# Kernel tuning notes

Hardware: AMD Instinct MI355X
Metric: run time of the kernel (lower is better)

The kernel has to match this reference:

```python
import jax, jax.numpy as jnp
import numpy as np
from functools import partial

EPS = 1e-5
SCALE = 2
NUM_BLOCKS = 2


def _layernorm(x, g, b):
    mu = jnp.mean(x, axis=-1, keepdims=True)
    var = jnp.var(x, axis=-1, keepdims=True)
    return (x - mu) * jax.lax.rsqrt(var + EPS) * g + b


def _rwkv(tokens, td, Wk, Wv, Wr, Wo, ln_g, ln_b):
    # tokens: (B, N, C)
    x = _layernorm(tokens, ln_g, ln_b)
    k = jnp.einsum('bnc,oc->bno', x, Wk)
    v = jnp.einsum('bnc,oc->bno', x, Wv)
    r = jax.nn.sigmoid(jnp.einsum('bnc,oc->bno', x, Wr))
    decay = jnp.exp(-jax.nn.relu(td))  # (C,)

    def step(state, inp):
        kt, vt, rt = inp  # each (B, C)
        state = state * decay + kt
        return state, rt * (state + vt)

    B, N, C = tokens.shape
    init = jnp.zeros((B, C), dtype=tokens.dtype)
    # scan over token axis
    _, yT = jax.lax.scan(step, init, (k.transpose(1, 0, 2), v.transpose(1, 0, 2), r.transpose(1, 0, 2)))
    y = yT.transpose(1, 0, 2)  # (B, N, C)
    return jnp.einsum('bnc,oc->bno', y, Wo)


def reference(x, global_state, cond_gw, cond_gb, cond_bw, cond_bb,
              td, Wk, Wv, Wr, Wo, ln_g, ln_b, gp_w, gp_b, bp_w, bp_b):
    B, C, H, W = x.shape
    Hp, Wp = H * SCALE, W * SCALE
    # bilinear upsample, half-pixel centers == torch align_corners=False
    x_up = jax.image.resize(x, (B, C, Hp, Wp), method='bilinear')
    tokens = x_up.reshape(B, C, Hp * Wp).transpose(0, 2, 1)  # (B, N, C)
    # semantic conditioning (FiLM from global state)
    gamma = (global_state @ cond_gw.T + cond_gb)[:, None, :]
    beta = (global_state @ cond_bw.T + cond_bb)[:, None, :]
    tokens = tokens * (1.0 + gamma) + beta

    out = x_up
    cur = tokens
    for i in range(NUM_BLOCKS):
        if i > 0:
            cur = out.reshape(B, C, Hp * Wp).transpose(0, 2, 1)
        t = _rwkv(cur, td[i], Wk[i], Wv[i], Wr[i], Wo[i], ln_g[i], ln_b[i])
        g = jnp.einsum('bnc,oc->bno', t, gp_w[i]) + gp_b[i]
        bt = jnp.einsum('bnc,oc->bno', t, bp_w[i]) + bp_b[i]
        g = g.transpose(0, 2, 1).reshape(B, C, Hp, Wp)
        bt = bt.transpose(0, 2, 1).reshape(B, C, Hp, Wp)
        out = out * (1.0 + jnp.tanh(g)) + bt
    return out


def setup_inputs() -> dict:
    key = jax.random.key(0)
    ks = jax.random.split(key, 16)
    B, C, H, W = 8, 128, 64, 64
    w_scale = 0.02
    inp = {
        'x': jax.random.normal(ks[0], (B, C, H, W), jnp.float32),
        'global_state': jax.random.normal(ks[1], (B, C), jnp.float32),
        'cond_gw': jax.random.normal(ks[2], (C, C), jnp.float32) * w_scale,
        'cond_gb': jnp.zeros((C,), jnp.float32),
        'cond_bw': jax.random.normal(ks[3], (C, C), jnp.float32) * w_scale,
        'cond_bb': jnp.zeros((C,), jnp.float32),
        'td': jax.random.uniform(ks[4], (NUM_BLOCKS, C), jnp.float32),
        'Wk': jax.random.normal(ks[5], (NUM_BLOCKS, C, C), jnp.float32) * w_scale,
        'Wv': jax.random.normal(ks[6], (NUM_BLOCKS, C, C), jnp.float32) * w_scale,
        'Wr': jax.random.normal(ks[7], (NUM_BLOCKS, C, C), jnp.float32) * w_scale,
        'Wo': jax.random.normal(ks[8], (NUM_BLOCKS, C, C), jnp.float32) * w_scale,
        'ln_g': jnp.ones((NUM_BLOCKS, C), jnp.float32),
        'ln_b': jnp.zeros((NUM_BLOCKS, C), jnp.float32),
        'gp_w': jax.random.normal(ks[9], (NUM_BLOCKS, C, C), jnp.float32) * w_scale,
        'gp_b': jnp.zeros((NUM_BLOCKS, C), jnp.float32),
        'bp_w': jax.random.normal(ks[10], (NUM_BLOCKS, C, C), jnp.float32) * w_scale,
        'bp_b': jnp.zeros((NUM_BLOCKS, C), jnp.float32),
    }
    return inp
```

## Files before the change

kernel.cpp:

```cpp
#include <hip/hip_runtime.h>
#include <hip/hip_bf16.h>

#define BB 8
#define CC 128
#define NN 16384
#define MM (BB * NN)
#define NCH 64
#define CLN 256

typedef __attribute__((ext_vector_type(8))) short short8;
typedef __attribute__((ext_vector_type(4))) float floatx4;
typedef unsigned short u16;
typedef unsigned int u32;

__device__ __forceinline__ float bf2f(u16 h) {
  u32 u = ((u32)h) << 16;
  return __builtin_bit_cast(float, u);
}
__device__ __forceinline__ u16 f2bf(float f) {
  u32 u = __builtin_bit_cast(u32, f);
  u32 r = u + 0x7FFFu + ((u >> 16) & 1u);
  return (u16)(r >> 16);
}

__global__ void film_kernel(const float* __restrict__ gs, const float* __restrict__ gw,
                            const float* __restrict__ gb, const float* __restrict__ bw,
                            const float* __restrict__ bb, float* __restrict__ gamma,
                            float* __restrict__ beta) {
  int idx = blockIdx.x * 256 + threadIdx.x;
  int b = idx >> 7, c = idx & 127;
  float sg = 0.f, sb = 0.f;
  for (int j = 0; j < 128; ++j) {
    float g = gs[b * 128 + j];
    sg += g * gw[c * 128 + j];
    sb += g * bw[c * 128 + j];
  }
  gamma[idx] = sg + gb[c];
  beta[idx] = sb + bb[c];
}

__global__ void convert_kernel(const float* __restrict__ Wk, const float* __restrict__ Wv,
                               const float* __restrict__ Wr, const float* __restrict__ Wo,
                               const float* __restrict__ gp, const float* __restrict__ bp,
                               u16* __restrict__ dst) {
  int idx = blockIdx.x * 256 + threadIdx.x;
  int which = idx >> 15;
  int off = idx & 32767;
  const float* s;
  switch (which) {
    case 0: s = Wk; break; case 1: s = Wv; break; case 2: s = Wr; break;
    case 3: s = Wo; break; case 4: s = gp; break; default: s = bp; break;
  }
  dst[idx] = f2bf(s[off]);
}

template <int UPS>
__global__ __launch_bounds__(256) void prep_kernel(
    const float* __restrict__ src, const float* __restrict__ gamma,
    const float* __restrict__ beta, const float* __restrict__ lng,
    const float* __restrict__ lnb, float* __restrict__ outp, u16* __restrict__ xn) {
  __shared__ float tile[64][129];
  __shared__ float smu[64], srs[64];
  int bidx = blockIdx.x;
  int half = bidx & 1;
  int ho = (bidx >> 1) & 127;
  int b = bidx >> 8;
  int wo0 = half * 64;
  int tid = threadIdx.x;
  int tk = tid & 63;
  int wo = wo0 + tk;
  int c0 = tid >> 6;
  int j0 = 0, j1 = 0, i0 = 0, i1 = 0;
  float wy0 = 0.f, wy1 = 0.f, wx0 = 0.f, wx1 = 0.f;
  if (UPS) {
    int jj = ho >> 1;
    if ((ho & 1) == 0) { j0 = jj > 0 ? jj - 1 : 0; j1 = jj; wy0 = 0.25f; wy1 = 0.75f; }
    else               { j0 = jj; j1 = jj < 63 ? jj + 1 : 63; wy0 = 0.75f; wy1 = 0.25f; }
    int ii = wo >> 1;
    if ((wo & 1) == 0) { i0 = ii > 0 ? ii - 1 : 0; i1 = ii; wx0 = 0.25f; wx1 = 0.75f; }
    else               { i0 = ii; i1 = ii < 63 ? ii + 1 : 63; wx0 = 0.75f; wx1 = 0.25f; }
  }
  for (int it = 0; it < 32; ++it) {
    int c = it * 4 + c0;
    float v;
    if (UPS) {
      const float* xp = src + ((size_t)(b * 128 + c)) * 4096;
      v = wy0 * (wx0 * xp[j0 * 64 + i0] + wx1 * xp[j0 * 64 + i1]) +
          wy1 * (wx0 * xp[j1 * 64 + i0] + wx1 * xp[j1 * 64 + i1]);
      outp[((size_t)(b * 128 + c)) * 16384 + ho * 128 + wo] = v;
      v = v * (1.f + gamma[b * 128 + c]) + beta[b * 128 + c];
    } else {
      v = src[((size_t)(b * 128 + c)) * 16384 + ho * 128 + wo];
    }
    tile[tk][c] = v;
  }
  __syncthreads();
  {
    int token = tid >> 2, q = tid & 3;
    float s = 0.f, s2 = 0.f;
    for (int j = 0; j < 32; ++j) { float v = tile[token][q * 32 + j]; s += v; s2 += v * v; }
    s += __shfl_xor(s, 1); s2 += __shfl_xor(s2, 1);
    s += __shfl_xor(s, 2); s2 += __shfl_xor(s2, 2);
    if (q == 0) {
      float mu = s * 0.0078125f;
      float var = s2 * 0.0078125f - mu * mu;
      smu[token] = mu;
      srs[token] = rsqrtf(var + 1e-5f);
    }
  }
  __syncthreads();
  size_t base = ((size_t)b * 16384 + ho * 128 + wo0) * 128;
  for (int it = 0; it < 32; ++it) {
    int idx = it * 256 + tid;
    int token = idx >> 7, c = idx & 127;
    float v = (tile[token][c] - smu[token]) * srs[token] * lng[c] + lnb[c];
    xn[base + idx] = f2bf(v);
  }
}

template <int MODE>
__global__ __launch_bounds__(256) void gemm_rowout_kernel(
    const u16* __restrict__ A, const u16* __restrict__ W0, const u16* __restrict__ W1,
    const u16* __restrict__ W2, float* __restrict__ outK, u16* __restrict__ outV,
    u16* __restrict__ outR) {
  __shared__ u16 Alds[128 * 128];
  __shared__ u16 Wlds[128 * 128];
  int tid = threadIdx.x;
  int wave = tid >> 6, lane = tid & 63;
  int l15 = lane & 15, l4 = lane >> 4;
  size_t row0 = (size_t)blockIdx.x * 128;
#pragma unroll
  for (int it = 0; it < 8; ++it) {
    int idx = it * 256 + tid;
    int r = idx >> 4, s = idx & 15;
    uint4 d = *(const uint4*)(A + (row0 + r) * 128 + s * 8);
    *(uint4*)(&Alds[r * 128 + ((s ^ (r & 15)) << 3)]) = d;
  }
  const u16* Wsarr[3] = {W0, W1, W2};
  const int NW = (MODE == 0) ? 3 : 1;
#pragma unroll
  for (int wsi = 0; wsi < NW; ++wsi) {
#pragma unroll
    for (int it = 0; it < 8; ++it) {
      int idx = it * 256 + tid;
      int r = idx >> 4, s = idx & 15;
      uint4 d = *(const uint4*)(Wsarr[wsi] + r * 128 + s * 8);
      *(uint4*)(&Wlds[r * 128 + ((s ^ (r & 15)) << 3)]) = d;
    }
    __syncthreads();
    floatx4 acc[2][8];
#pragma unroll
    for (int mi = 0; mi < 2; ++mi)
#pragma unroll
      for (int ni = 0; ni < 8; ++ni) acc[mi][ni] = (floatx4){0.f, 0.f, 0.f, 0.f};
#pragma unroll
    for (int kk = 0; kk < 4; ++kk) {
      int seg = kk * 4 + l4;
      short8 a0 = *(const short8*)(&Alds[(wave * 32 + l15) * 128 + ((seg ^ l15) << 3)]);
      short8 a1 = *(const short8*)(&Alds[(wave * 32 + 16 + l15) * 128 + ((seg ^ l15) << 3)]);
#pragma unroll
      for (int ni = 0; ni < 8; ++ni) {
        short8 bfr = *(const short8*)(&Wlds[(ni * 16 + l15) * 128 + ((seg ^ l15) << 3)]);
        acc[0][ni] = __builtin_amdgcn_mfma_f32_16x16x32_bf16(a0, bfr, acc[0][ni], 0, 0, 0);
        acc[1][ni] = __builtin_amdgcn_mfma_f32_16x16x32_bf16(a1, bfr, acc[1][ni], 0, 0, 0);
      }
    }
#pragma unroll
    for (int mi = 0; mi < 2; ++mi) {
#pragma unroll
      for (int ni = 0; ni < 8; ++ni) {
        int col = ni * 16 + l15;
#pragma unroll
        for (int j = 0; j < 4; ++j) {
          size_t row = row0 + wave * 32 + mi * 16 + l4 * 4 + j;
          float val = acc[mi][ni][j];
          if (MODE == 0) {
            if (wsi == 0) outK[row * 128 + col] = val;
            else if (wsi == 1) outV[row * 128 + col] = f2bf(val);
            else outR[row * 128 + col] = f2bf(1.f / (1.f + __expf(-val)));
          } else {
            outV[row * 128 + col] = f2bf(val);
          }
        }
      }
    }
    __syncthreads();
  }
}

__global__ __launch_bounds__(256) void scan1_kernel(const float* __restrict__ k,
                                                    const float* __restrict__ td,
                                                    float* __restrict__ S) {
  int tid = blockIdx.x * 256 + threadIdx.x;
  int c = tid & 127;
  int b = (tid >> 7) & 7;
  int chunk = tid >> 10;
  float d = __expf(-fmaxf(td[c], 0.f));
  const float* kp = k + ((size_t)b * 16384 + chunk * 256) * 128 + c;
  float s = 0.f;
#pragma unroll 16
  for (int t = 0; t < CLN; ++t) s = s * d + kp[(size_t)t * 128];
  S[chunk * 1024 + b * 128 + c] = s;
}

__global__ __launch_bounds__(256) void scan2_kernel(const float* __restrict__ S,
                                                    const float* __restrict__ td,
                                                    float* __restrict__ init) {
  int wave = threadIdx.x >> 6, lane = threadIdx.x & 63;
  int bc = blockIdx.x * 4 + wave;
  int c = bc & 127;
  float a = __expf(-fmaxf(td[c], 0.f) * 256.f);
  float s = S[lane * 1024 + bc];
  for (int off = 1; off < 64; off <<= 1) {
    float sp = __shfl_up(s, off);
    float ap = __shfl_up(a, off);
    if (lane >= off) { s = s + a * sp; a = a * ap; }
  }
  float e = __shfl_up(s, 1);
  if (lane == 0) e = 0.f;
  init[lane * 1024 + bc] = e;
}

__global__ __launch_bounds__(256) void scan3_kernel(const float* __restrict__ k,
                                                    u16* __restrict__ v,
                                                    const u16* __restrict__ r,
                                                    const float* __restrict__ init,
                                                    const float* __restrict__ td) {
  int tid = blockIdx.x * 256 + threadIdx.x;
  int c = tid & 127;
  int b = (tid >> 7) & 7;
  int chunk = tid >> 10;
  float d = __expf(-fmaxf(td[c], 0.f));
  float s = init[chunk * 1024 + b * 128 + c];
  size_t base = ((size_t)b * 16384 + chunk * 256) * 128 + c;
  const float* kp = k + base;
  u16* vp = v + base;
  const u16* rp = r + base;
#pragma unroll 8
  for (int t = 0; t < CLN; ++t) {
    size_t o = (size_t)t * 128;
    s = s * d + kp[o];
    float vv = bf2f(vp[o]);
    float rv = bf2f(rp[o]);
    vp[o] = f2bf(rv * (s + vv));
  }
}

__global__ __launch_bounds__(512) void blend_kernel(
    const u16* __restrict__ t, const u16* __restrict__ Wg, const u16* __restrict__ Wb,
    const float* __restrict__ gpb, const float* __restrict__ bpb,
    float* __restrict__ outp) {
  __shared__ u16 T[128 * 128];
  int tid = threadIdx.x;
  int b = blockIdx.x >> 7;
  int tok0 = (blockIdx.x & 127) * 128;
#pragma unroll
  for (int it = 0; it < 4; ++it) {
    int idx = it * 512 + tid;
    int r = idx >> 4, s = idx & 15;
    uint4 d = *(const uint4*)(t + ((size_t)(b * 16384 + tok0 + r)) * 128 + s * 8);
    *(uint4*)(&T[r * 128 + ((s ^ (r & 15)) << 3)]) = d;
  }
  int wave = tid >> 6, lane = tid & 63;
  int l15 = lane & 15, l4 = lane >> 4;
  int ob = (wave & 3) * 32;
  int tb = (wave >> 2) * 64;
  short8 wg[2][4], wb2[2][4];
#pragma unroll
  for (int mi = 0; mi < 2; ++mi)
#pragma unroll
    for (int kk = 0; kk < 4; ++kk) {
      int o = ob + mi * 16 + l15;
      wg[mi][kk] = *(const short8*)(Wg + o * 128 + kk * 32 + l4 * 8);
      wb2[mi][kk] = *(const short8*)(Wb + o * 128 + kk * 32 + l4 * 8);
    }
  __syncthreads();
  floatx4 ag[2][4], ab[2][4];
#pragma unroll
  for (int mi = 0; mi < 2; ++mi)
#pragma unroll
    for (int ni = 0; ni < 4; ++ni) {
      ag[mi][ni] = (floatx4){0.f, 0.f, 0.f, 0.f};
      ab[mi][ni] = (floatx4){0.f, 0.f, 0.f, 0.f};
    }
#pragma unroll
  for (int kk = 0; kk < 4; ++kk) {
    int seg = kk * 4 + l4;
#pragma unroll
    for (int ni = 0; ni < 4; ++ni) {
      short8 tf = *(const short8*)(&T[(tb + ni * 16 + l15) * 128 + ((seg ^ l15) << 3)]);
#pragma unroll
      for (int mi = 0; mi < 2; ++mi) {
        ag[mi][ni] = __builtin_amdgcn_mfma_f32_16x16x32_bf16(wg[mi][kk], tf, ag[mi][ni], 0, 0, 0);
        ab[mi][ni] = __builtin_amdgcn_mfma_f32_16x16x32_bf16(wb2[mi][kk], tf, ab[mi][ni], 0, 0, 0);
      }
    }
  }
#pragma unroll
  for (int mi = 0; mi < 2; ++mi) {
#pragma unroll
    for (int ni = 0; ni < 4; ++ni) {
      int tok = tok0 + tb + ni * 16 + l15;
#pragma unroll
      for (int j = 0; j < 4; ++j) {
        int o = ob + mi * 16 + l4 * 4 + j;
        size_t addr = ((size_t)(b * 128 + o)) * 16384 + tok;
        float g = ag[mi][ni][j] + gpb[o];
        float bt = ab[mi][ni][j] + bpb[o];
        float prev = outp[addr];
        outp[addr] = prev * (1.f + tanhf(g)) + bt;
      }
    }
  }
}

extern "C" void kernel_launch(void* const* d_in, const int* in_sizes, int n_in,
                              void* d_out, int out_size, void* d_ws, size_t ws_size,
                              hipStream_t stream) {
  const float* x        = (const float*)d_in[0];
  const float* gs       = (const float*)d_in[1];
  const float* cond_gw  = (const float*)d_in[2];
  const float* cond_gb  = (const float*)d_in[3];
  const float* cond_bw  = (const float*)d_in[4];
  const float* cond_bb  = (const float*)d_in[5];
  const float* td       = (const float*)d_in[6];
  const float* Wk       = (const float*)d_in[7];
  const float* Wv       = (const float*)d_in[8];
  const float* Wr       = (const float*)d_in[9];
  const float* Wo       = (const float*)d_in[10];
  const float* ln_g     = (const float*)d_in[11];
  const float* ln_b     = (const float*)d_in[12];
  const float* gp_w     = (const float*)d_in[13];
  const float* gp_b     = (const float*)d_in[14];
  const float* bp_w     = (const float*)d_in[15];
  const float* bp_b     = (const float*)d_in[16];
  float* outp = (float*)d_out;

  char* w = (char*)d_ws;
  float* gamma = (float*)w; w += 4096;
  float* beta  = (float*)w; w += 4096;
  u16* wbf     = (u16*)w;   w += 6 * 2 * 16384 * sizeof(u16);
  u16* xn      = (u16*)w;   w += (size_t)MM * 128 * sizeof(u16);
  float* kbuf  = (float*)w; w += (size_t)MM * 128 * sizeof(float);
  u16* vbuf    = (u16*)w;   w += (size_t)MM * 128 * sizeof(u16);
  u16* rbuf    = (u16*)w;   w += (size_t)MM * 128 * sizeof(u16);
  float* Sbuf  = (float*)w; w += NCH * 1024 * sizeof(float);
  float* ibuf  = (float*)w; w += NCH * 1024 * sizeof(float);

  film_kernel<<<4, 256, 0, stream>>>(gs, cond_gw, cond_gb, cond_bw, cond_bb, gamma, beta);
  convert_kernel<<<768, 256, 0, stream>>>(Wk, Wv, Wr, Wo, gp_w, bp_w, wbf);

  for (int blk = 0; blk < 2; ++blk) {
    const u16* bWk = wbf + 0 * 32768 + blk * 16384;
    const u16* bWv = wbf + 1 * 32768 + blk * 16384;
    const u16* bWr = wbf + 2 * 32768 + blk * 16384;
    const u16* bWo = wbf + 3 * 32768 + blk * 16384;
    const u16* bGp = wbf + 4 * 32768 + blk * 16384;
    const u16* bBp = wbf + 5 * 32768 + blk * 16384;
    const float* tdi = td + blk * 128;

    if (blk == 0)
      prep_kernel<1><<<2048, 256, 0, stream>>>(x, gamma, beta, ln_g, ln_b, outp, xn);
    else
      prep_kernel<0><<<2048, 256, 0, stream>>>(outp, nullptr, nullptr, ln_g + 128,
                                               ln_b + 128, nullptr, xn);

    gemm_rowout_kernel<0><<<1024, 256, 0, stream>>>(xn, bWk, bWv, bWr, kbuf, vbuf, rbuf);
    scan1_kernel<<<256, 256, 0, stream>>>(kbuf, tdi, Sbuf);
    scan2_kernel<<<256, 256, 0, stream>>>(Sbuf, tdi, ibuf);
    scan3_kernel<<<256, 256, 0, stream>>>(kbuf, vbuf, rbuf, ibuf, tdi);
    gemm_rowout_kernel<1><<<1024, 256, 0, stream>>>(vbuf, bWo, nullptr, nullptr,
                                                    nullptr, xn, nullptr);
    blend_kernel<<<1024, 512, 0, stream>>>(xn, bGp, bBp, gp_b + blk * 128,
                                           bp_b + blk * 128, outp);
  }
}
```

Baseline: 331.5 us.

## Fuse scan pass, Wo GEMM and gated blend into one tail kernel

Merges the final scan pass, the Wo projection and the gamma/beta blend into one kernel per 128-token chunk, keeping y and t in LDS instead of writing them to global memory. Stores k in bf16 instead of fp32 and halves the scan chunk length to 128, with scan2 combining chunk pairs so its 64-lane prefix still covers 128 chunks. The blend now writes the NCHW output with coalesced vectorized accesses through an LDS transpose. In exchange, only half the threads do the serial scan inside each block. Precision drops because k is now bf16 and the tanh multiplier and bias are rounded to bf16 before the blend.

```diff
diff --git a/kernel.cpp b/kernel.cpp
--- a/kernel.cpp
+++ b/kernel.cpp
@@ -5,8 +5,8 @@
 #define CC 128
 #define NN 16384
 #define MM (BB * NN)
-#define NCH 64
-#define CLN 256
+#define NCH 128
+#define CLN 128
 
 typedef __attribute__((ext_vector_type(8))) short short8;
 typedef __attribute__((ext_vector_type(4))) float floatx4;
@@ -118,10 +118,9 @@
   }
 }
 
-template <int MODE>
-__global__ __launch_bounds__(256) void gemm_rowout_kernel(
+__global__ __launch_bounds__(256) void gemm_kvr_kernel(
     const u16* __restrict__ A, const u16* __restrict__ W0, const u16* __restrict__ W1,
-    const u16* __restrict__ W2, float* __restrict__ outK, u16* __restrict__ outV,
+    const u16* __restrict__ W2, u16* __restrict__ outK, u16* __restrict__ outV,
     u16* __restrict__ outR) {
   __shared__ u16 Alds[128 * 128];
   __shared__ u16 Wlds[128 * 128];
@@ -132,20 +131,19 @@
 #pragma unroll
   for (int it = 0; it < 8; ++it) {
     int idx = it * 256 + tid;
-    int r = idx >> 4, s = idx & 15;
-    uint4 d = *(const uint4*)(A + (row0 + r) * 128 + s * 8);
-    *(uint4*)(&Alds[r * 128 + ((s ^ (r & 15)) << 3)]) = d;
+    int rr = idx >> 4, s = idx & 15;
+    uint4 d = *(const uint4*)(A + (row0 + rr) * 128 + s * 8);
+    *(uint4*)(&Alds[rr * 128 + ((s ^ (rr & 15)) << 3)]) = d;
   }
   const u16* Wsarr[3] = {W0, W1, W2};
-  const int NW = (MODE == 0) ? 3 : 1;
-#pragma unroll
-  for (int wsi = 0; wsi < NW; ++wsi) {
+#pragma unroll
+  for (int wsi = 0; wsi < 3; ++wsi) {
 #pragma unroll
     for (int it = 0; it < 8; ++it) {
       int idx = it * 256 + tid;
-      int r = idx >> 4, s = idx & 15;
-      uint4 d = *(const uint4*)(Wsarr[wsi] + r * 128 + s * 8);
-      *(uint4*)(&Wlds[r * 128 + ((s ^ (r & 15)) << 3)]) = d;
+      int rr = idx >> 4, s = idx & 15;
+      uint4 d = *(const uint4*)(Wsarr[wsi] + rr * 128 + s * 8);
+      *(uint4*)(&Wlds[rr * 128 + ((s ^ (rr & 15)) << 3)]) = d;
     }
     __syncthreads();
     floatx4 acc[2][8];
@@ -174,13 +172,9 @@
         for (int j = 0; j < 4; ++j) {
           size_t row = row0 + wave * 32 + mi * 16 + l4 * 4 + j;
           float val = acc[mi][ni][j];
-          if (MODE == 0) {
-            if (wsi == 0) outK[row * 128 + col] = val;
-            else if (wsi == 1) outV[row * 128 + col] = f2bf(val);
-            else outR[row * 128 + col] = f2bf(1.f / (1.f + __expf(-val)));
-          } else {
-            outV[row * 128 + col] = f2bf(val);
-          }
+          if (wsi == 0) outK[row * 128 + col] = f2bf(val);
+          else if (wsi == 1) outV[row * 128 + col] = f2bf(val);
+          else outR[row * 128 + col] = f2bf(1.f / (1.f + __expf(-val)));
         }
       }
     }
@@ -188,7 +182,7 @@
   }
 }
 
-__global__ __launch_bounds__(256) void scan1_kernel(const float* __restrict__ k,
+__global__ __launch_bounds__(256) void scan1_kernel(const u16* __restrict__ k,
                                                     const float* __restrict__ td,
                                                     float* __restrict__ S) {
   int tid = blockIdx.x * 256 + threadIdx.x;
@@ -196,10 +190,10 @@
   int b = (tid >> 7) & 7;
   int chunk = tid >> 10;
   float d = __expf(-fmaxf(td[c], 0.f));
-  const float* kp = k + ((size_t)b * 16384 + chunk * 256) * 128 + c;
+  const u16* kp = k + ((size_t)b * 16384 + chunk * 128) * 128 + c;
   float s = 0.f;
 #pragma unroll 16
-  for (int t = 0; t < CLN; ++t) s = s * d + kp[(size_t)t * 128];
+  for (int t = 0; t < CLN; ++t) s = s * d + bf2f(kp[(size_t)t * 128]);
   S[chunk * 1024 + b * 128 + c] = s;
 }
 
@@ -209,77 +203,105 @@
   int wave = threadIdx.x >> 6, lane = threadIdx.x & 63;
   int bc = blockIdx.x * 4 + wave;
   int c = bc & 127;
-  float a = __expf(-fmaxf(td[c], 0.f) * 256.f);
-  float s = S[lane * 1024 + bc];
+  float a1 = __expf(-fmaxf(td[c], 0.f) * 128.f);
+  float s0 = S[(2 * lane) * 1024 + bc];
+  float s1 = S[(2 * lane + 1) * 1024 + bc];
+  float s = s1 + a1 * s0;
+  float a = a1 * a1;
   for (int off = 1; off < 64; off <<= 1) {
-    float sp = __shfl_up(s, off);
-    float ap = __shfl_up(a, off);
-    if (lane >= off) { s = s + a * sp; a = a * ap; }
+    float ss = __shfl_up(s, off);
+    float aa = __shfl_up(a, off);
+    if (lane >= off) { s = s + a * ss; a = a * aa; }
   }
   float e = __shfl_up(s, 1);
   if (lane == 0) e = 0.f;
-  init[lane * 1024 + bc] = e;
-}
-
-__global__ __launch_bounds__(256) void scan3_kernel(const float* __restrict__ k,
-                                                    u16* __restrict__ v,
-                                                    const u16* __restrict__ r,
-                                                    const float* __restrict__ init,
-                                                    const float* __restrict__ td) {
-  int tid = blockIdx.x * 256 + threadIdx.x;
-  int c = tid & 127;
-  int b = (tid >> 7) & 7;
-  int chunk = tid >> 10;
-  float d = __expf(-fmaxf(td[c], 0.f));
-  float s = init[chunk * 1024 + b * 128 + c];
-  size_t base = ((size_t)b * 16384 + chunk * 256) * 128 + c;
-  const float* kp = k + base;
-  u16* vp = v + base;
-  const u16* rp = r + base;
-#pragma unroll 8
-  for (int t = 0; t < CLN; ++t) {
-    size_t o = (size_t)t * 128;
-    s = s * d + kp[o];
-    float vv = bf2f(vp[o]);
-    float rv = bf2f(rp[o]);
-    vp[o] = f2bf(rv * (s + vv));
-  }
-}
-
-__global__ __launch_bounds__(512) void blend_kernel(
-    const u16* __restrict__ t, const u16* __restrict__ Wg, const u16* __restrict__ Wb,
+  init[(2 * lane) * 1024 + bc] = e;
+  init[(2 * lane + 1) * 1024 + bc] = a1 * e + s0;
+}
+
+__global__ __launch_bounds__(256) void tail_kernel(
+    const u16* __restrict__ k, const u16* __restrict__ v, const u16* __restrict__ r,
+    const float* __restrict__ init, const float* __restrict__ td,
+    const u16* __restrict__ Wo, const u16* __restrict__ Wg, const u16* __restrict__ Wb,
     const float* __restrict__ gpb, const float* __restrict__ bpb,
     float* __restrict__ outp) {
-  __shared__ u16 T[128 * 128];
+  __shared__ u32 SMEM[16384];
+  u16* Y  = (u16*)SMEM;
+  u16* T2 = ((u16*)SMEM) + 16384;
+  u32* MB = SMEM;
+
   int tid = threadIdx.x;
-  int b = blockIdx.x >> 7;
-  int tok0 = (blockIdx.x & 127) * 128;
-#pragma unroll
-  for (int it = 0; it < 4; ++it) {
-    int idx = it * 512 + tid;
-    int r = idx >> 4, s = idx & 15;
-    uint4 d = *(const uint4*)(t + ((size_t)(b * 16384 + tok0 + r)) * 128 + s * 8);
-    *(uint4*)(&T[r * 128 + ((s ^ (r & 15)) << 3)]) = d;
-  }
   int wave = tid >> 6, lane = tid & 63;
   int l15 = lane & 15, l4 = lane >> 4;
-  int ob = (wave & 3) * 32;
-  int tb = (wave >> 2) * 64;
-  short8 wg[2][4], wb2[2][4];
+  int b = blockIdx.x >> 7;
+  int chunk = blockIdx.x & 127;
+  size_t ebase = ((size_t)b * 16384 + (size_t)chunk * 128) * 128;
+
+  int ob = wave * 32;
+  short8 wof[2][4], wgf[2][4], wbf2[2][4];
 #pragma unroll
   for (int mi = 0; mi < 2; ++mi)
 #pragma unroll
     for (int kk = 0; kk < 4; ++kk) {
       int o = ob + mi * 16 + l15;
-      wg[mi][kk] = *(const short8*)(Wg + o * 128 + kk * 32 + l4 * 8);
-      wb2[mi][kk] = *(const short8*)(Wb + o * 128 + kk * 32 + l4 * 8);
-    }
-  __syncthreads();
-  floatx4 ag[2][4], ab[2][4];
+      wof[mi][kk]  = *(const short8*)(Wo + o * 128 + kk * 32 + l4 * 8);
+      wgf[mi][kk]  = *(const short8*)(Wg + o * 128 + kk * 32 + l4 * 8);
+      wbf2[mi][kk] = *(const short8*)(Wb + o * 128 + kk * 32 + l4 * 8);
+    }
+
+  if (tid < 128) {
+    int c = tid;
+    float d = __expf(-fmaxf(td[c], 0.f));
+    float s = init[chunk * 1024 + b * 128 + c];
+    const u16* kp = k + ebase + c;
+    const u16* vp = v + ebase + c;
+    const u16* rp = r + ebase + c;
+    int seg = c >> 3, cl = c & 7;
+#pragma unroll 8
+    for (int t = 0; t < 128; ++t) {
+      s = s * d + bf2f(kp[(size_t)t * 128]);
+      float y = bf2f(rp[(size_t)t * 128]) * (s + bf2f(vp[(size_t)t * 128]));
+      Y[t * 128 + (((seg ^ (t & 15)) << 3) | cl)] = f2bf(y);
+    }
+  }
+  __syncthreads();
+
+  floatx4 acc[2][8];
 #pragma unroll
   for (int mi = 0; mi < 2; ++mi)
 #pragma unroll
-    for (int ni = 0; ni < 4; ++ni) {
+    for (int ni = 0; ni < 8; ++ni) acc[mi][ni] = (floatx4){0.f, 0.f, 0.f, 0.f};
+#pragma unroll
+  for (int kk = 0; kk < 4; ++kk) {
+    int seg = kk * 4 + l4;
+#pragma unroll
+    for (int ni = 0; ni < 8; ++ni) {
+      short8 yf = *(const short8*)(&Y[(ni * 16 + l15) * 128 + ((seg ^ l15) << 3)]);
+#pragma unroll
+      for (int mi = 0; mi < 2; ++mi)
+        acc[mi][ni] = __builtin_amdgcn_mfma_f32_16x16x32_bf16(wof[mi][kk], yf, acc[mi][ni], 0, 0, 0);
+    }
+  }
+#pragma unroll
+  for (int mi = 0; mi < 2; ++mi)
+#pragma unroll
+    for (int ni = 0; ni < 8; ++ni) {
+      int tok = ni * 16 + l15;
+#pragma unroll
+      for (int j = 0; j < 4; j += 2) {
+        int o = ob + mi * 16 + l4 * 4 + j;
+        u32 pack = (u32)f2bf(acc[mi][ni][j]) | ((u32)f2bf(acc[mi][ni][j + 1]) << 16);
+        int pos = tok * 128 + ((((o >> 3) ^ (tok & 15)) << 3) | (o & 7));
+        *(u32*)(T2 + pos) = pack;
+      }
+    }
+  __syncthreads();
+
+  floatx4 ag[2][8], ab[2][8];
+#pragma unroll
+  for (int mi = 0; mi < 2; ++mi)
+#pragma unroll
+    for (int ni = 0; ni < 8; ++ni) {
       ag[mi][ni] = (floatx4){0.f, 0.f, 0.f, 0.f};
       ab[mi][ni] = (floatx4){0.f, 0.f, 0.f, 0.f};
     }
@@ -287,30 +309,54 @@
   for (int kk = 0; kk < 4; ++kk) {
     int seg = kk * 4 + l4;
 #pragma unroll
-    for (int ni = 0; ni < 4; ++ni) {
-      short8 tf = *(const short8*)(&T[(tb + ni * 16 + l15) * 128 + ((seg ^ l15) << 3)]);
+    for (int ni = 0; ni < 8; ++ni) {
+      short8 tf = *(const short8*)(&T2[(ni * 16 + l15) * 128 + ((seg ^ l15) << 3)]);
 #pragma unroll
       for (int mi = 0; mi < 2; ++mi) {
-        ag[mi][ni] = __builtin_amdgcn_mfma_f32_16x16x32_bf16(wg[mi][kk], tf, ag[mi][ni], 0, 0, 0);
-        ab[mi][ni] = __builtin_amdgcn_mfma_f32_16x16x32_bf16(wb2[mi][kk], tf, ab[mi][ni], 0, 0, 0);
+        ag[mi][ni] = __builtin_amdgcn_mfma_f32_16x16x32_bf16(wgf[mi][kk], tf, ag[mi][ni], 0, 0, 0);
+        ab[mi][ni] = __builtin_amdgcn_mfma_f32_16x16x32_bf16(wbf2[mi][kk], tf, ab[mi][ni], 0, 0, 0);
       }
     }
   }
-#pragma unroll
-  for (int mi = 0; mi < 2; ++mi) {
-#pragma unroll
-    for (int ni = 0; ni < 4; ++ni) {
-      int tok = tok0 + tb + ni * 16 + l15;
+  __syncthreads();
+
+#pragma unroll
+  for (int mi = 0; mi < 2; ++mi)
+#pragma unroll
+    for (int ni = 0; ni < 8; ++ni) {
+      int tok = ni * 16 + l15;
 #pragma unroll
       for (int j = 0; j < 4; ++j) {
         int o = ob + mi * 16 + l4 * 4 + j;
-        size_t addr = ((size_t)(b * 128 + o)) * 16384 + tok;
         float g = ag[mi][ni][j] + gpb[o];
+        float m = 1.f + tanhf(g);
         float bt = ab[mi][ni][j] + bpb[o];
-        float prev = outp[addr];
-        outp[addr] = prev * (1.f + tanhf(g)) + bt;
+        MB[o * 128 + ((((tok >> 3) ^ (o & 15)) << 3) | (tok & 7))] =
+            (u32)f2bf(m) | ((u32)f2bf(bt) << 16);
       }
     }
+  __syncthreads();
+
+#pragma unroll
+  for (int it = 0; it < 8; ++it) {
+    int idx = it * 256 + tid;
+    int o = idx >> 4, seg = idx & 15;
+    int sp = ((seg ^ (o & 15)) << 3);
+    uint4 mb0 = *(const uint4*)(&MB[o * 128 + sp]);
+    uint4 mb1 = *(const uint4*)(&MB[o * 128 + sp + 4]);
+    float* op = outp + ((size_t)(b * 128 + o)) * 16384 + chunk * 128 + seg * 8;
+    float4 o0 = *(float4*)op;
+    float4 o1 = *(float4*)(op + 4);
+    o0.x = o0.x * bf2f((u16)(mb0.x & 0xffff)) + bf2f((u16)(mb0.x >> 16));
+    o0.y = o0.y * bf2f((u16)(mb0.y & 0xffff)) + bf2f((u16)(mb0.y >> 16));
+    o0.z = o0.z * bf2f((u16)(mb0.z & 0xffff)) + bf2f((u16)(mb0.z >> 16));
+    o0.w = o0.w * bf2f((u16)(mb0.w & 0xffff)) + bf2f((u16)(mb0.w >> 16));
+    o1.x = o1.x * bf2f((u16)(mb1.x & 0xffff)) + bf2f((u16)(mb1.x >> 16));
+    o1.y = o1.y * bf2f((u16)(mb1.y & 0xffff)) + bf2f((u16)(mb1.y >> 16));
+    o1.z = o1.z * bf2f((u16)(mb1.z & 0xffff)) + bf2f((u16)(mb1.z >> 16));
+    o1.w = o1.w * bf2f((u16)(mb1.w & 0xffff)) + bf2f((u16)(mb1.w >> 16));
+    *(float4*)op = o0;
+    *(float4*)(op + 4) = o1;
   }
 }
 
@@ -341,7 +387,7 @@
   float* beta  = (float*)w; w += 4096;
   u16* wbf     = (u16*)w;   w += 6 * 2 * 16384 * sizeof(u16);
   u16* xn      = (u16*)w;   w += (size_t)MM * 128 * sizeof(u16);
-  float* kbuf  = (float*)w; w += (size_t)MM * 128 * sizeof(float);
+  u16* kbuf    = (u16*)w;   w += (size_t)MM * 128 * sizeof(u16);
   u16* vbuf    = (u16*)w;   w += (size_t)MM * 128 * sizeof(u16);
   u16* rbuf    = (u16*)w;   w += (size_t)MM * 128 * sizeof(u16);
   float* Sbuf  = (float*)w; w += NCH * 1024 * sizeof(float);
@@ -365,13 +411,11 @@
       prep_kernel<0><<<2048, 256, 0, stream>>>(outp, nullptr, nullptr, ln_g + 128,
                                                ln_b + 128, nullptr, xn);
 
-    gemm_rowout_kernel<0><<<1024, 256, 0, stream>>>(xn, bWk, bWv, bWr, kbuf, vbuf, rbuf);
-    scan1_kernel<<<256, 256, 0, stream>>>(kbuf, tdi, Sbuf);
+    gemm_kvr_kernel<<<1024, 256, 0, stream>>>(xn, bWk, bWv, bWr, kbuf, vbuf, rbuf);
+    scan1_kernel<<<512, 256, 0, stream>>>(kbuf, tdi, Sbuf);
     scan2_kernel<<<256, 256, 0, stream>>>(Sbuf, tdi, ibuf);
-    scan3_kernel<<<256, 256, 0, stream>>>(kbuf, vbuf, rbuf, ibuf, tdi);
-    gemm_rowout_kernel<1><<<1024, 256, 0, stream>>>(vbuf, bWo, nullptr, nullptr,
-                                                    nullptr, xn, nullptr);
-    blend_kernel<<<1024, 512, 0, stream>>>(xn, bGp, bBp, gp_b + blk * 128,
-                                           bp_b + blk * 128, outp);
-  }
-}
+    tail_kernel<<<1024, 256, 0, stream>>>(kbuf, vbuf, rbuf, ibuf, tdi,
+                                          bWo, bGp, bBp, gp_b + blk * 128,
+                                          bp_b + blk * 128, outp);
+  }
+}
```

New measurement: 339.0 us. 2.3% more time.
